# Kernel optimization log

Measured on AMD Instinct MI355X. Metric: run time of the kernel, lower is better.

The kernel has to match this reference:

```python
import jax, jax.numpy as jnp
import numpy as np

B, N, D_IN, D_HID, D_OUT = 8192, 32, 512, 512, 512


def setup_inputs() -> dict:
    key = jax.random.key(0)
    ks = jax.random.split(key, 5)
    scale_mlp = (6.0 / (D_IN + D_HID)) ** 0.5
    scale_out = (6.0 / (D_HID + D_OUT)) ** 0.5
    return {
        "self_vecs": jax.random.normal(ks[0], (B, D_IN), dtype=jnp.float32),
        "neigh_vecs": jax.random.normal(ks[1], (B, N, D_IN), dtype=jnp.float32),
        "mlp_w": jax.random.uniform(ks[2], (D_IN, D_HID), jnp.float32, -scale_mlp, scale_mlp),
        "mlp_b": jnp.zeros((D_HID,), dtype=jnp.float32),
        "neigh_w": jax.random.uniform(ks[3], (D_HID, D_OUT), jnp.float32, -scale_out, scale_out),
        "self_w": jax.random.uniform(ks[4], (D_IN, D_OUT), jnp.float32, -scale_out, scale_out),
    }


def reference(self_vecs, neigh_vecs, mlp_w, mlp_b, neigh_w, self_w):
    # per-neighbor MLP: [B,N,D_in] @ [D_in,D_hid] + b, relu (dropout=0)
    h = jax.nn.relu(jnp.einsum('bni,ih->bnh', neigh_vecs, mlp_w) + mlp_b)
    # max-pool over neighbors -> [B, D_hid]
    pooled = jnp.max(h, axis=1)
    from_neighs = pooled @ neigh_w          # [B, D_out]
    from_self = self_vecs @ self_w          # [B, D_out]
    return jax.nn.relu(from_self + from_neighs)
```

## Files before the change

### kernel.cpp

```cpp
#include <hip/hip_runtime.h>
#include <hip/hip_bf16.h>
#include <stdint.h>

#define D 512

typedef __attribute__((ext_vector_type(8))) short short8_t;
typedef __attribute__((ext_vector_type(4))) float floatx4;

static __device__ __forceinline__ unsigned short f2bf(float f) {
    union { __hip_bfloat16 h; unsigned short u; } c;
    c.h = __float2bfloat16(f);
    return c.u;
}

static __device__ __forceinline__ void ld_lds16(const void* g, void* l) {
    __builtin_amdgcn_global_load_lds(
        (const __attribute__((address_space(1))) void*)g,
        (__attribute__((address_space(3))) void*)l, 16, 0, 0);
}

__global__ void __launch_bounds__(256) prep_weights(
    const float* __restrict__ w1, const float* __restrict__ w2,
    const float* __restrict__ w3,
    unsigned short* __restrict__ w1t, unsigned short* __restrict__ w2t,
    unsigned short* __restrict__ w3t)
{
    int idx = blockIdx.x * 256 + threadIdx.x;
    int m = idx >> 18;
    int i = idx & 262143;
    int k = i >> 9, n = i & 511;
    const float* src = (m == 0) ? w1 : (m == 1) ? w2 : w3;
    unsigned short* dst = (m == 0) ? w1t : (m == 1) ? w2t : w3t;
    dst[n * D + k] = f2bf(src[i]);
}

__global__ void __launch_bounds__(256) mlp_pool_kernel(
    const float* __restrict__ neigh,
    const unsigned short* __restrict__ w1t,
    const float* __restrict__ bias,
    unsigned short* __restrict__ pooled)
{
    __shared__ __align__(16) float As[64 * 64];
    __shared__ __align__(16) short Bs[256 * 64];
    __shared__ float pool_s[2][256];

    const int tid  = threadIdx.x;
    const int wave = tid >> 6;
    const int lane = tid & 63;
    const int quad = lane >> 4;
    const int l15  = lane & 15;
    const int mw = (wave >> 1) * 32;
    const int nw = (wave & 1) * 128;

    const int m0 = (blockIdx.x >> 1) * 64;
    const int n0 = (blockIdx.x & 1) * 256;

    const float* agp[4];
#pragma unroll
    for (int rr = 0; rr < 4; ++rr) {
        int ci = wave * 256 + rr * 64 + lane;
        int r = ci >> 4, pos = ci & 15, ch = pos ^ (r & 15);
        agp[rr] = neigh + (size_t)(m0 + r) * D + ch * 4;
    }
    char* alp0 = (char*)As + wave * 4096 + lane * 16;
    const unsigned short* bgp0 = w1t +
        (size_t)(n0 + wave * 64 + (lane >> 3)) * D +
        ((lane & 7) ^ ((lane >> 3) & 7)) * 8;
    char* blp0 = (char*)Bs + wave * 8192 + lane * 16;

    floatx4 acc[2][8];
#pragma unroll
    for (int i = 0; i < 2; ++i)
#pragma unroll
        for (int j = 0; j < 8; ++j) acc[i][j] = (floatx4){0.f, 0.f, 0.f, 0.f};

    for (int kk = 0; kk < 8; ++kk) {
        const int k0 = kk * 64;
        __syncthreads();
#pragma unroll
        for (int rr = 0; rr < 4; ++rr)
            ld_lds16(agp[rr] + k0, alp0 + rr * 1024);
#pragma unroll
        for (int rr = 0; rr < 8; ++rr)
            ld_lds16(bgp0 + rr * 4096 + k0, blp0 + rr * 1024);
        __syncthreads();

#pragma unroll
        for (int s = 0; s < 2; ++s) {
            short8_t af[2], bf[8];
#pragma unroll
            for (int mt = 0; mt < 2; ++mt) {
                int r = mw + mt * 16 + l15;
                int c2 = s * 8 + quad * 2;
                floatx4 a0 = *(const floatx4*)(
                    (const char*)As + r * 256 + ((c2 ^ l15) * 16));
                floatx4 a1 = *(const floatx4*)(
                    (const char*)As + r * 256 + (((c2 + 1) ^ l15) * 16));
                short8_t v;
                v[0] = (short)f2bf(a0[0]); v[1] = (short)f2bf(a0[1]);
                v[2] = (short)f2bf(a0[2]); v[3] = (short)f2bf(a0[3]);
                v[4] = (short)f2bf(a1[0]); v[5] = (short)f2bf(a1[1]);
                v[6] = (short)f2bf(a1[2]); v[7] = (short)f2bf(a1[3]);
                af[mt] = v;
            }
#pragma unroll
            for (int nt = 0; nt < 8; ++nt) {
                int r = nw + nt * 16 + l15;
                int c = (s * 4 + quad) ^ (l15 & 7);
                bf[nt] = *(const short8_t*)((const char*)Bs + r * 128 + c * 16);
            }
#pragma unroll
            for (int mt = 0; mt < 2; ++mt)
#pragma unroll
                for (int nt = 0; nt < 8; ++nt)
                    acc[mt][nt] = __builtin_amdgcn_mfma_f32_16x16x32_bf16(
                        af[mt], bf[nt], acc[mt][nt], 0, 0, 0);
        }
    }

#pragma unroll
    for (int nt = 0; nt < 8; ++nt) {
        float v = -3.4e38f;
#pragma unroll
        for (int mt = 0; mt < 2; ++mt)
#pragma unroll
            for (int rg = 0; rg < 4; ++rg) v = fmaxf(v, acc[mt][nt][rg]);
        v = fmaxf(v, __shfl_xor(v, 16));
        v = fmaxf(v, __shfl_xor(v, 32));
        if (lane < 16) pool_s[wave >> 1][nw + nt * 16 + l15] = v;
    }
    __syncthreads();
#pragma unroll
    for (int it = 0; it < 2; ++it) {
        int i = it * 256 + tid;
        int g = i >> 8, col = i & 255;
        float v = fmaxf(pool_s[g][col] + bias[n0 + col], 0.0f);
        pooled[(size_t)((m0 >> 5) + g) * D + n0 + col] = f2bf(v);
    }
}

__global__ void __launch_bounds__(256) out_gemm_kernel(
    const unsigned short* __restrict__ pooled,
    const float* __restrict__ selfv,
    const unsigned short* __restrict__ w2t,
    const unsigned short* __restrict__ w3t,
    float* __restrict__ out)
{
    __shared__ __align__(16) short As[128 * 64];
    __shared__ __align__(16) short Bs[128 * 64];

    const int tid  = threadIdx.x;
    const int wave = tid >> 6;
    const int lane = tid & 63;
    const int quad = lane >> 4;
    const int l15  = lane & 15;
    const int mw = (wave >> 1) * 64;
    const int nw = (wave & 1) * 64;

    const int m0 = (blockIdx.x >> 2) * 128;
    const int n0 = (blockIdx.x & 3) * 128;

    floatx4 acc[4][4];
#pragma unroll
    for (int i = 0; i < 4; ++i)
#pragma unroll
        for (int j = 0; j < 4; ++j) acc[i][j] = (floatx4){0.f, 0.f, 0.f, 0.f};

    for (int kk = 0; kk < 16; ++kk) {
        const int k0 = (kk & 7) * 64;
        __syncthreads();
        if (kk < 8) {
#pragma unroll
            for (int rnd = 0; rnd < 4; ++rnd) {
                int l = rnd * 256 + tid;
                int r = l >> 3, g = l & 7;
                short8_t v = *reinterpret_cast<const short8_t*>(
                    pooled + (size_t)(m0 + r) * D + k0 + g * 8);
                *reinterpret_cast<short8_t*>(&As[r * 64 + ((g ^ (r & 7)) * 8)]) = v;
            }
#pragma unroll
            for (int rnd = 0; rnd < 4; ++rnd) {
                int l = rnd * 256 + tid;
                int r = l >> 3, g = l & 7;
                short8_t v = *reinterpret_cast<const short8_t*>(
                    w2t + (size_t)(n0 + r) * D + k0 + g * 8);
                *reinterpret_cast<short8_t*>(&Bs[r * 64 + ((g ^ (r & 7)) * 8)]) = v;
            }
        } else {
#pragma unroll
            for (int rnd = 0; rnd < 4; ++rnd) {
                int l = rnd * 256 + tid;
                int r = l >> 3, g = l & 7;
                const float4* src = reinterpret_cast<const float4*>(
                    selfv + (size_t)(m0 + r) * D + k0 + g * 8);
                float4 f0 = src[0];
                float4 f1 = src[1];
                short8_t v;
                v[0] = (short)f2bf(f0.x); v[1] = (short)f2bf(f0.y);
                v[2] = (short)f2bf(f0.z); v[3] = (short)f2bf(f0.w);
                v[4] = (short)f2bf(f1.x); v[5] = (short)f2bf(f1.y);
                v[6] = (short)f2bf(f1.z); v[7] = (short)f2bf(f1.w);
                *reinterpret_cast<short8_t*>(&As[r * 64 + ((g ^ (r & 7)) * 8)]) = v;
            }
#pragma unroll
            for (int rnd = 0; rnd < 4; ++rnd) {
                int l = rnd * 256 + tid;
                int r = l >> 3, g = l & 7;
                short8_t v = *reinterpret_cast<const short8_t*>(
                    w3t + (size_t)(n0 + r) * D + k0 + g * 8);
                *reinterpret_cast<short8_t*>(&Bs[r * 64 + ((g ^ (r & 7)) * 8)]) = v;
            }
        }
        __syncthreads();
#pragma unroll
        for (int s = 0; s < 2; ++s) {
            short8_t af[4], bfr[4];
#pragma unroll
            for (int mt = 0; mt < 4; ++mt) {
                int r = mw + mt * 16 + l15;
                int c = (s * 4 + quad) ^ (r & 7);
                af[mt] = *reinterpret_cast<const short8_t*>(&As[r * 64 + c * 8]);
            }
#pragma unroll
            for (int nt = 0; nt < 4; ++nt) {
                int r = nw + nt * 16 + l15;
                int c = (s * 4 + quad) ^ (r & 7);
                bfr[nt] = *reinterpret_cast<const short8_t*>(&Bs[r * 64 + c * 8]);
            }
#pragma unroll
            for (int mt = 0; mt < 4; ++mt)
#pragma unroll
                for (int nt = 0; nt < 4; ++nt)
                    acc[mt][nt] = __builtin_amdgcn_mfma_f32_16x16x32_bf16(
                        af[mt], bfr[nt], acc[mt][nt], 0, 0, 0);
        }
    }

#pragma unroll
    for (int mt = 0; mt < 4; ++mt)
#pragma unroll
        for (int nt = 0; nt < 4; ++nt)
#pragma unroll
            for (int rg = 0; rg < 4; ++rg) {
                int row = m0 + mw + mt * 16 + quad * 4 + rg;
                int col = n0 + nw + nt * 16 + l15;
                out[(size_t)row * D + col] = fmaxf(acc[mt][nt][rg], 0.0f);
            }
}

extern "C" void kernel_launch(void* const* d_in, const int* in_sizes, int n_in,
                              void* d_out, int out_size, void* d_ws, size_t ws_size,
                              hipStream_t stream) {
    const float* selfv = (const float*)d_in[0];
    const float* neigh = (const float*)d_in[1];
    const float* w1    = (const float*)d_in[2];
    const float* b1    = (const float*)d_in[3];
    const float* w2    = (const float*)d_in[4];
    const float* w3    = (const float*)d_in[5];
    float* out = (float*)d_out;

    unsigned short* pooled = (unsigned short*)d_ws;
    unsigned short* w1t = (unsigned short*)((char*)d_ws + 8388608);
    unsigned short* w2t = w1t + 262144;
    unsigned short* w3t = w2t + 262144;

    prep_weights<<<3072, 256, 0, stream>>>(w1, w2, w3, w1t, w2t, w3t);
    mlp_pool_kernel<<<8192, 256, 0, stream>>>(neigh, w1t, b1, pooled);
    out_gemm_kernel<<<256, 256, 0, stream>>>(pooled, selfv, w2t, w3t, out);
}
```

Baseline: 834.7 us.

## Double-buffer MLP-pool GEMM with 128-row tiles and register-staged bf16 A conversion

Restructures the neighbor MLP+maxpool kernel. It now uses 128x256 tiles with BK=32 and double-buffered LDS, prefetching the next K-slice while the current one runs on the MFMA units. The fp32 neighbor rows are loaded into registers and converted to bf16 once before being written to LDS, instead of being converted inside the inner loop on every read. It also adds a workgroup-index remap for locality, halves the grid, and sets launch bounds for 2 blocks per CU. The larger accumulator array raises register pressure, and there is one sync per K-step instead of two.

```diff
diff --git a/kernel.cpp b/kernel.cpp
--- a/kernel.cpp
+++ b/kernel.cpp
@@ -34,104 +34,145 @@
     dst[n * D + k] = f2bf(src[i]);
 }
 
-__global__ void __launch_bounds__(256) mlp_pool_kernel(
+#define BM 128
+#define BN 256
+#define BK 32
+
+__global__ void __launch_bounds__(256, 2) mlp_pool_kernel(
     const float* __restrict__ neigh,
     const unsigned short* __restrict__ w1t,
     const float* __restrict__ bias,
     unsigned short* __restrict__ pooled)
 {
-    __shared__ __align__(16) float As[64 * 64];
-    __shared__ __align__(16) short Bs[256 * 64];
-    __shared__ float pool_s[2][256];
+    __shared__ __align__(16) short As[2][BM * BK];
+    __shared__ __align__(16) short Bs[2][BN * BK];
+    __shared__ float pool_s[4][256];
 
     const int tid  = threadIdx.x;
     const int wave = tid >> 6;
     const int lane = tid & 63;
     const int quad = lane >> 4;
     const int l15  = lane & 15;
-    const int mw = (wave >> 1) * 32;
+    const int mw = (wave >> 1) * 64;
     const int nw = (wave & 1) * 128;
 
-    const int m0 = (blockIdx.x >> 1) * 64;
-    const int n0 = (blockIdx.x & 1) * 256;
-
-    const float* agp[4];
-#pragma unroll
-    for (int rr = 0; rr < 4; ++rr) {
-        int ci = wave * 256 + rr * 64 + lane;
-        int r = ci >> 4, pos = ci & 15, ch = pos ^ (r & 15);
-        agp[rr] = neigh + (size_t)(m0 + r) * D + ch * 4;
-    }
-    char* alp0 = (char*)As + wave * 4096 + lane * 16;
-    const unsigned short* bgp0 = w1t +
-        (size_t)(n0 + wave * 64 + (lane >> 3)) * D +
-        ((lane & 7) ^ ((lane >> 3) & 7)) * 8;
-    char* blp0 = (char*)Bs + wave * 8192 + lane * 16;
-
-    floatx4 acc[2][8];
-#pragma unroll
-    for (int i = 0; i < 2; ++i)
+    const int wgid = (blockIdx.x & 7) * 512 + (blockIdx.x >> 3);
+    const int m0 = (wgid >> 1) * BM;
+    const int n0 = (wgid & 1) * BN;
+
+    const int ar = tid >> 2, apos = tid & 3;
+    const float* a_src0 = neigh + (size_t)(m0 + ar) * D + apos * 8;
+    const int a_off0 = ar * BK + ((apos ^ (ar & 3)) * 8);
+
+    const int bci = wave * 256 + lane;
+    const int br = bci >> 2, bpos = bci & 3;
+    const unsigned short* b_src0 =
+        w1t + (size_t)(n0 + br) * D + ((bpos ^ (br & 3)) * 8);
+    const int bdst_byte0 = bci * 16;
+
+    int aoff[4], boff[8];
+#pragma unroll
+    for (int mt = 0; mt < 4; ++mt) {
+        int r = mw + mt * 16 + l15;
+        aoff[mt] = r * BK + ((quad ^ (r & 3)) * 8);
+    }
+#pragma unroll
+    for (int nt = 0; nt < 8; ++nt) {
+        int r = nw + nt * 16 + l15;
+        boff[nt] = r * BK + ((quad ^ (r & 3)) * 8);
+    }
+
+    floatx4 acc[4][8];
+#pragma unroll
+    for (int i = 0; i < 4; ++i)
 #pragma unroll
         for (int j = 0; j < 8; ++j) acc[i][j] = (floatx4){0.f, 0.f, 0.f, 0.f};
 
-    for (int kk = 0; kk < 8; ++kk) {
-        const int k0 = kk * 64;
+#pragma unroll
+    for (int rr = 0; rr < 4; ++rr)
+        ld_lds16(b_src0 + rr * (16 * D),
+                 (char*)&Bs[0][0] + bdst_byte0 + rr * 1024);
+#pragma unroll
+    for (int rnd = 0; rnd < 2; ++rnd) {
+        const float4* s = (const float4*)(a_src0 + rnd * (64 * D));
+        float4 f0 = s[0], f1 = s[1];
+        short8_t v;
+        v[0] = (short)f2bf(f0.x); v[1] = (short)f2bf(f0.y);
+        v[2] = (short)f2bf(f0.z); v[3] = (short)f2bf(f0.w);
+        v[4] = (short)f2bf(f1.x); v[5] = (short)f2bf(f1.y);
+        v[6] = (short)f2bf(f1.z); v[7] = (short)f2bf(f1.w);
+        *(short8_t*)&As[0][a_off0 + rnd * (64 * BK)] = v;
+    }
+    __syncthreads();
+
+    int cur = 0;
+    for (int kk = 0; kk < 16; ++kk) {
+        const int nxt = cur ^ 1;
+        float4 f0[2], f1[2];
+        if (kk < 15) {
+            const int ko = (kk + 1) * BK;
+#pragma unroll
+            for (int rnd = 0; rnd < 2; ++rnd) {
+                const float4* s = (const float4*)(a_src0 + rnd * (64 * D) + ko);
+                f0[rnd] = s[0];
+                f1[rnd] = s[1];
+            }
+#pragma unroll
+            for (int rr = 0; rr < 4; ++rr)
+                ld_lds16(b_src0 + rr * (16 * D) + ko,
+                         (char*)&Bs[nxt][0] + bdst_byte0 + rr * 1024);
+        }
+
+        short8_t af[4], bf[8];
+#pragma unroll
+        for (int mt = 0; mt < 4; ++mt)
+            af[mt] = *(const short8_t*)&As[cur][aoff[mt]];
+#pragma unroll
+        for (int nt = 0; nt < 8; ++nt)
+            bf[nt] = *(const short8_t*)&Bs[cur][boff[nt]];
+#pragma unroll
+        for (int mt = 0; mt < 4; ++mt)
+#pragma unroll
+            for (int nt = 0; nt < 8; ++nt)
+                acc[mt][nt] = __builtin_amdgcn_mfma_f32_16x16x32_bf16(
+                    af[mt], bf[nt], acc[mt][nt], 0, 0, 0);
+
+        if (kk < 15) {
+#pragma unroll
+            for (int rnd = 0; rnd < 2; ++rnd) {
+                short8_t v;
+                v[0] = (short)f2bf(f0[rnd].x); v[1] = (short)f2bf(f0[rnd].y);
+                v[2] = (short)f2bf(f0[rnd].z); v[3] = (short)f2bf(f0[rnd].w);
+                v[4] = (short)f2bf(f1[rnd].x); v[5] = (short)f2bf(f1[rnd].y);
+                v[6] = (short)f2bf(f1[rnd].z); v[7] = (short)f2bf(f1[rnd].w);
+                *(short8_t*)&As[nxt][a_off0 + rnd * (64 * BK)] = v;
+            }
+        }
         __syncthreads();
-#pragma unroll
-        for (int rr = 0; rr < 4; ++rr)
-            ld_lds16(agp[rr] + k0, alp0 + rr * 1024);
-#pragma unroll
-        for (int rr = 0; rr < 8; ++rr)
-            ld_lds16(bgp0 + rr * 4096 + k0, blp0 + rr * 1024);
-        __syncthreads();
-
-#pragma unroll
-        for (int s = 0; s < 2; ++s) {
-            short8_t af[2], bf[8];
-#pragma unroll
-            for (int mt = 0; mt < 2; ++mt) {
-                int r = mw + mt * 16 + l15;
-                int c2 = s * 8 + quad * 2;
-                floatx4 a0 = *(const floatx4*)(
-                    (const char*)As + r * 256 + ((c2 ^ l15) * 16));
-                floatx4 a1 = *(const floatx4*)(
-                    (const char*)As + r * 256 + (((c2 + 1) ^ l15) * 16));
-                short8_t v;
-                v[0] = (short)f2bf(a0[0]); v[1] = (short)f2bf(a0[1]);
-                v[2] = (short)f2bf(a0[2]); v[3] = (short)f2bf(a0[3]);
-                v[4] = (short)f2bf(a1[0]); v[5] = (short)f2bf(a1[1]);
-                v[6] = (short)f2bf(a1[2]); v[7] = (short)f2bf(a1[3]);
-                af[mt] = v;
-            }
-#pragma unroll
-            for (int nt = 0; nt < 8; ++nt) {
-                int r = nw + nt * 16 + l15;
-                int c = (s * 4 + quad) ^ (l15 & 7);
-                bf[nt] = *(const short8_t*)((const char*)Bs + r * 128 + c * 16);
-            }
-#pragma unroll
-            for (int mt = 0; mt < 2; ++mt)
-#pragma unroll
-                for (int nt = 0; nt < 8; ++nt)
-                    acc[mt][nt] = __builtin_amdgcn_mfma_f32_16x16x32_bf16(
-                        af[mt], bf[nt], acc[mt][nt], 0, 0, 0);
-        }
+        cur = nxt;
     }
 
 #pragma unroll
     for (int nt = 0; nt < 8; ++nt) {
-        float v = -3.4e38f;
-#pragma unroll
-        for (int mt = 0; mt < 2; ++mt)
-#pragma unroll
-            for (int rg = 0; rg < 4; ++rg) v = fmaxf(v, acc[mt][nt][rg]);
-        v = fmaxf(v, __shfl_xor(v, 16));
-        v = fmaxf(v, __shfl_xor(v, 32));
-        if (lane < 16) pool_s[wave >> 1][nw + nt * 16 + l15] = v;
+        float v0 = -3.4e38f, v1 = -3.4e38f;
+#pragma unroll
+        for (int rg = 0; rg < 4; ++rg) {
+            v0 = fmaxf(v0, fmaxf(acc[0][nt][rg], acc[1][nt][rg]));
+            v1 = fmaxf(v1, fmaxf(acc[2][nt][rg], acc[3][nt][rg]));
+        }
+        v0 = fmaxf(v0, __shfl_xor(v0, 16));
+        v0 = fmaxf(v0, __shfl_xor(v0, 32));
+        v1 = fmaxf(v1, __shfl_xor(v1, 16));
+        v1 = fmaxf(v1, __shfl_xor(v1, 32));
+        if (lane < 16) {
+            const int g = (wave >> 1) * 2;
+            pool_s[g][nw + nt * 16 + l15]     = v0;
+            pool_s[g + 1][nw + nt * 16 + l15] = v1;
+        }
     }
     __syncthreads();
 #pragma unroll
-    for (int it = 0; it < 2; ++it) {
+    for (int it = 0; it < 4; ++it) {
         int i = it * 256 + tid;
         int g = i >> 8, col = i & 255;
         float v = fmaxf(pool_s[g][col] + bias[n0 + col], 0.0f);
@@ -146,8 +187,8 @@
     const unsigned short* __restrict__ w3t,
     float* __restrict__ out)
 {
-    __shared__ __align__(16) short As[128 * 64];
-    __shared__ __align__(16) short Bs[128 * 64];
+    __shared__ __align__(16) short As2[128 * 64];
+    __shared__ __align__(16) short Bs2[128 * 64];
 
     const int tid  = threadIdx.x;
     const int wave = tid >> 6;
@@ -176,7 +217,7 @@
                 int r = l >> 3, g = l & 7;
                 short8_t v = *reinterpret_cast<const short8_t*>(
                     pooled + (size_t)(m0 + r) * D + k0 + g * 8);
-                *reinterpret_cast<short8_t*>(&As[r * 64 + ((g ^ (r & 7)) * 8)]) = v;
+                *reinterpret_cast<short8_t*>(&As2[r * 64 + ((g ^ (r & 7)) * 8)]) = v;
             }
 #pragma unroll
             for (int rnd = 0; rnd < 4; ++rnd) {
@@ -184,7 +225,7 @@
                 int r = l >> 3, g = l & 7;
                 short8_t v = *reinterpret_cast<const short8_t*>(
                     w2t + (size_t)(n0 + r) * D + k0 + g * 8);
-                *reinterpret_cast<short8_t*>(&Bs[r * 64 + ((g ^ (r & 7)) * 8)]) = v;
+                *reinterpret_cast<short8_t*>(&Bs2[r * 64 + ((g ^ (r & 7)) * 8)]) = v;
             }
         } else {
 #pragma unroll
@@ -200,7 +241,7 @@
                 v[2] = (short)f2bf(f0.z); v[3] = (short)f2bf(f0.w);
                 v[4] = (short)f2bf(f1.x); v[5] = (short)f2bf(f1.y);
                 v[6] = (short)f2bf(f1.z); v[7] = (short)f2bf(f1.w);
-                *reinterpret_cast<short8_t*>(&As[r * 64 + ((g ^ (r & 7)) * 8)]) = v;
+                *reinterpret_cast<short8_t*>(&As2[r * 64 + ((g ^ (r & 7)) * 8)]) = v;
             }
 #pragma unroll
             for (int rnd = 0; rnd < 4; ++rnd) {
@@ -208,7 +249,7 @@
                 int r = l >> 3, g = l & 7;
                 short8_t v = *reinterpret_cast<const short8_t*>(
                     w3t + (size_t)(n0 + r) * D + k0 + g * 8);
-                *reinterpret_cast<short8_t*>(&Bs[r * 64 + ((g ^ (r & 7)) * 8)]) = v;
+                *reinterpret_cast<short8_t*>(&Bs2[r * 64 + ((g ^ (r & 7)) * 8)]) = v;
             }
         }
         __syncthreads();
@@ -219,13 +260,13 @@
             for (int mt = 0; mt < 4; ++mt) {
                 int r = mw + mt * 16 + l15;
                 int c = (s * 4 + quad) ^ (r & 7);
-                af[mt] = *reinterpret_cast<const short8_t*>(&As[r * 64 + c * 8]);
+                af[mt] = *reinterpret_cast<const short8_t*>(&As2[r * 64 + c * 8]);
             }
 #pragma unroll
             for (int nt = 0; nt < 4; ++nt) {
                 int r = nw + nt * 16 + l15;
                 int c = (s * 4 + quad) ^ (r & 7);
-                bfr[nt] = *reinterpret_cast<const short8_t*>(&Bs[r * 64 + c * 8]);
+                bfr[nt] = *reinterpret_cast<const short8_t*>(&Bs2[r * 64 + c * 8]);
             }
 #pragma unroll
             for (int mt = 0; mt < 4; ++mt)
@@ -265,6 +306,6 @@
     unsigned short* w3t = w2t + 262144;
 
     prep_weights<<<3072, 256, 0, stream>>>(w1, w2, w3, w1t, w2t, w3t);
-    mlp_pool_kernel<<<8192, 256, 0, stream>>>(neigh, w1t, b1, pooled);
+    mlp_pool_kernel<<<4096, 256, 0, stream>>>(neigh, w1t, b1, pooled);
     out_gemm_kernel<<<256, 256, 0, stream>>>(pooled, selfv, w2t, w3t, out);
 }
```

After: 878.2 us. +5.2%, slower.
